# Kernel optimization log

Measured on AMD Instinct MI355X. Metric: run time of the kernel, lower is better.

The kernel has to match this reference:

```python
import jax, jax.numpy as jnp
import numpy as np

K = 3
STRIDE = 1
PAD = 1
DIL = 1


def conv2d(x, w, b, stride, pad, dil):
    y = jax.lax.conv_general_dilated(
        x, w, (stride, stride), [(pad, pad), (pad, pad)],
        rhs_dilation=(dil, dil), dimension_numbers=("NCHW", "OIHW", "NCHW"))
    return y + b[None, :, None, None]


def bilinear_gather(img, ys, xs):
    # img: (C,H,W); ys,xs: (KK,Ho,Wo) pixel coords.
    # grid_sample(mode=bilinear, padding_mode=zeros, align_corners=True):
    # out-of-range corners contribute 0, interpolation weights unchanged.
    H, W = img.shape[-2:]
    y0 = jnp.floor(ys)
    x0 = jnp.floor(xs)
    wy1 = ys - y0
    wx1 = xs - x0
    wy0 = 1.0 - wy1
    wx0 = 1.0 - wx1

    def g(yc, xc):
        yi = yc.astype(jnp.int32)
        xi = xc.astype(jnp.int32)
        valid = (yi >= 0) & (yi < H) & (xi >= 0) & (xi < W)
        yi = jnp.clip(yi, 0, H - 1)
        xi = jnp.clip(xi, 0, W - 1)
        v = img[:, yi, xi]  # (C,KK,Ho,Wo)
        return v * valid[None].astype(img.dtype)

    return (g(y0, x0) * (wy0 * wx0)[None]
            + g(y0, x0 + 1.0) * (wy0 * wx1)[None]
            + g(y0 + 1.0, x0) * (wy1 * wx0)[None]
            + g(y0 + 1.0, x0 + 1.0) * (wy1 * wx1)[None])


def setup_inputs() -> dict:
    key = jax.random.key(0)
    ks = jax.random.split(key, 4)
    B, C_in, H, W = 8, 64, 96, 96
    C_out = 64
    x = jax.random.normal(ks[0], (B, C_in, H, W), dtype=jnp.float32)
    weight = jax.random.normal(ks[1], (C_out, C_in, K, K), dtype=jnp.float32) * 0.05
    bias = jax.random.normal(ks[2], (C_out,), dtype=jnp.float32) * 0.01
    off_w = jax.random.normal(ks[3], (2 * K * K, C_in, K, K), dtype=jnp.float32) * 0.05
    off_b = jnp.zeros((2 * K * K,), dtype=jnp.float32)
    return {"x": x, "weight": weight, "bias": bias, "off_w": off_w, "off_b": off_b}


def reference(x, weight, bias, off_w, off_b):
    B, C, H, W = x.shape
    Ho = (H + 2 * PAD - DIL * (K - 1) - 1) // STRIDE + 1
    Wo = (W + 2 * PAD - DIL * (K - 1) - 1) // STRIDE + 1

    offsets = conv2d(x, off_w, off_b, STRIDE, PAD, DIL)  # (B,2*K*K,Ho,Wo)
    off = offsets.reshape(B, K * K, 2, Ho, Wo)

    # Base sampling grid (note: original code does NOT subtract padding; kept faithful).
    by, bx = jnp.meshgrid(jnp.arange(Ho, dtype=x.dtype), jnp.arange(Wo, dtype=x.dtype), indexing="ij")
    by = by * STRIDE + (K // 2) * DIL
    bx = bx * STRIDE + (K // 2) * DIL
    ko = jnp.arange(-(K // 2), K // 2 + 1, dtype=x.dtype)
    ky, kx = jnp.meshgrid(ko, ko, indexing="ij")

    sy = by[None, None] + ky.reshape(1, -1, 1, 1) + off[:, :, 0]  # (B,KK,Ho,Wo)
    sx = bx[None, None] + kx.reshape(1, -1, 1, 1) + off[:, :, 1]

    sampled = jax.vmap(bilinear_gather)(x, sy, sx)  # (B,C,KK,Ho,Wo)

    wflat = weight.reshape(weight.shape[0], C, K * K)  # (O,C,KK)
    out = jnp.einsum("bckhw,ock->bohw", sampled, wflat)
    return out + bias[None, :, None, None]
```

## Files before the change

### kernel.cpp

```cpp
#include <hip/hip_runtime.h>
#include <hip/hip_bf16.h>

#define HH 96
#define WW 96
#define HW 9216
#define NB 8

typedef __bf16 bf16x8 __attribute__((ext_vector_type(8)));
typedef float  f32x4  __attribute__((ext_vector_type(4)));

union BF8 { uint4 u; bf16x8 v; unsigned short s[8]; };

__device__ __forceinline__ unsigned short f2bf_bits(float f) {
    unsigned u = __float_as_uint(f);
    unsigned r = u + 0x7FFFu + ((u >> 16) & 1u);
    return (unsigned short)(r >> 16);
}
__device__ __forceinline__ float bf2f(unsigned short s) {
    return __uint_as_float(((unsigned)s) << 16);
}
__device__ __forceinline__ unsigned pkbf(float a, float b) {
    union { __hip_bfloat162 h; unsigned u; } c;
    c.h = __float22bfloat162_rn(make_float2(a, b));
    return c.u;
}

__device__ __forceinline__ void bl_setup(int h, int w, int r, int s, float oy, float ox,
                                         int* a, float* wg) {
    float sy = (float)(h + r) + oy;
    float sx = (float)(w + s) + ox;
    float fy = floorf(sy), fx = floorf(sx);
    int   y0 = (int)fy, x0 = (int)fx;
    int   y1 = y0 + 1, x1 = x0 + 1;
    float wy1 = sy - fy, wx1 = sx - fx;
    float wy0 = 1.f - wy1, wx0 = 1.f - wx1;
    float m00 = (y0 >= 0 && y0 < HH && x0 >= 0 && x0 < WW) ? 1.f : 0.f;
    float m01 = (y0 >= 0 && y0 < HH && x1 >= 0 && x1 < WW) ? 1.f : 0.f;
    float m10 = (y1 >= 0 && y1 < HH && x0 >= 0 && x0 < WW) ? 1.f : 0.f;
    float m11 = (y1 >= 0 && y1 < HH && x1 >= 0 && x1 < WW) ? 1.f : 0.f;
    int cy0 = min(max(y0, 0), HH - 1), cy1 = min(max(y1, 0), HH - 1);
    int cx0 = min(max(x0, 0), WW - 1), cx1 = min(max(x1, 0), WW - 1);
    a[0] = (cy0 * WW + cx0) * 64;  a[1] = (cy0 * WW + cx1) * 64;
    a[2] = (cy1 * WW + cx0) * 64;  a[3] = (cy1 * WW + cx1) * 64;
    wg[0] = wy0 * wx0 * m00;  wg[1] = wy0 * wx1 * m01;
    wg[2] = wy1 * wx0 * m10;  wg[3] = wy1 * wx1 * m11;
}

__global__ __launch_bounds__(256) void xcvt_prep(const float* __restrict__ x,
                                                 const float* __restrict__ weight,
                                                 const float* __restrict__ off_w,
                                                 unsigned short* __restrict__ xt,
                                                 unsigned short* __restrict__ wTb2,
                                                 unsigned short* __restrict__ owTb2) {
    __shared__ unsigned short T[64 * 64];
    int bid   = blockIdx.x;
    int t     = threadIdx.x;
    int b     = bid & 7;
    int pbase = (bid >> 3) * 64;
    int pl    = t & 63;
    int q     = t >> 6;

    const float* xp = x + ((size_t)(b * 64 + q * 16)) * HW + pbase + pl;
    unsigned short hb[16];
#pragma unroll
    for (int i = 0; i < 16; ++i) hb[i] = f2bf_bits(xp[(size_t)i * HW]);

    uint4 w0, w1;
    w0.x = hb[0]  | (hb[1]  << 16); w0.y = hb[2]  | (hb[3]  << 16);
    w0.z = hb[4]  | (hb[5]  << 16); w0.w = hb[6]  | (hb[7]  << 16);
    w1.x = hb[8]  | (hb[9]  << 16); w1.y = hb[10] | (hb[11] << 16);
    w1.z = hb[12] | (hb[13] << 16); w1.w = hb[14] | (hb[15] << 16);
    int sw = pl & 7;
    *(uint4*)&T[pl * 64 + (((2 * q)     ^ sw) << 3)] = w0;
    *(uint4*)&T[pl * 64 + (((2 * q + 1) ^ sw) << 3)] = w1;
    __syncthreads();

    int row = t >> 2, rs = row & 7;
    uint4 a  = *(const uint4*)&T[row * 64 + ((((t & 3) * 2)     ^ rs) << 3)];
    uint4 b2 = *(const uint4*)&T[row * 64 + ((((t & 3) * 2 + 1) ^ rs) << 3)];
    unsigned short* dst = xt + ((size_t)(b * HW + pbase)) * 64 + t * 16;
    *(uint4*)dst       = a;
    *(uint4*)(dst + 8) = b2;

    if (bid < 216) {
        int i = bid * 256 + t;
        if (i < 36864) {
            int ch = i & 7, lnn = (i >> 3) & 15, qdd = (i >> 7) & 3;
            int kc = (i >> 9) & 1, ct = (i >> 10) & 3, tap = i >> 12;
            int co = ct * 16 + lnn;
            int c  = kc * 32 + qdd * 8 + ch;
            wTb2[i] = f2bf_bits(weight[(co * 64 + c) * 9 + tap]);
        } else {
            int f = i - 36864;
            int ch = f & 7, lnn = (f >> 3) & 15, qdd = (f >> 7) & 3;
            int kc = (f >> 9) & 1, jt = (f >> 10) & 1, tap = f >> 11;
            int j = jt * 16 + lnn;
            int c = kc * 32 + qdd * 8 + ch;
            owTb2[f] = (j < 18) ? f2bf_bits(off_w[(j * 64 + c) * 9 + tap]) : (unsigned short)0;
        }
    }
}

__global__ __launch_bounds__(256) void deform_all(const unsigned short* __restrict__ xt,
                                                  const unsigned short* __restrict__ wTb2,
                                                  const unsigned short* __restrict__ owTb2,
                                                  const float* __restrict__ bias,
                                                  const float* __restrict__ ob,
                                                  float* __restrict__ out) {
    __shared__ float offs[4][16 * 20];

    int bid   = blockIdx.x;
    int t     = threadIdx.x;
    int b     = bid & 7;
    int wv    = t >> 6;
    int l     = t & 63;
    int ln    = l & 15;
    int qd    = l >> 4;
    int pbase = (bid >> 3) * 64 + wv * 16;
    int px    = pbase + ln;
    int h     = px / WW, w = px - h * WW;

    const unsigned short* xb = xt + (size_t)b * HW * 64;

    f32x4 aj0 = {0.f, 0.f, 0.f, 0.f};
    f32x4 aj1 = {0.f, 0.f, 0.f, 0.f};
#pragma unroll
    for (int tap = 0; tap < 9; ++tap) {
        int  r  = tap / 3, s = tap - r * 3;
        int  iy = h - 1 + r, ix = w - 1 + s;
        bool vd = (iy >= 0) & (iy < HH) & (ix >= 0) & (ix < WW);
        int  rec = (min(max(iy, 0), HH - 1) * WW + min(max(ix, 0), WW - 1)) * 64;
        BF8 a0, a1;
        a0.u = *(const uint4*)(xb + rec + qd * 8);
        a1.u = *(const uint4*)(xb + rec + 32 + qd * 8);
        if (!vd) { a0.u = make_uint4(0,0,0,0); a1.u = make_uint4(0,0,0,0); }

        const unsigned short* base0 = owTb2 + (size_t)tap * 2048 + l * 8;
        BF8 b00, b01, b10, b11;
        b00.u = *(const uint4*)(base0);
        b01.u = *(const uint4*)(base0 + 512);
        b10.u = *(const uint4*)(base0 + 1024);
        b11.u = *(const uint4*)(base0 + 1536);
        aj0 = __builtin_amdgcn_mfma_f32_16x16x32_bf16(a0.v, b00.v, aj0, 0, 0, 0);
        aj0 = __builtin_amdgcn_mfma_f32_16x16x32_bf16(a1.v, b01.v, aj0, 0, 0, 0);
        aj1 = __builtin_amdgcn_mfma_f32_16x16x32_bf16(a0.v, b10.v, aj1, 0, 0, 0);
        aj1 = __builtin_amdgcn_mfma_f32_16x16x32_bf16(a1.v, b11.v, aj1, 0, 0, 0);
    }

    {
        float* ow_ = offs[wv];
        float  obj = ob[ln];
#pragma unroll
        for (int rg = 0; rg < 4; ++rg) ow_[(qd * 4 + rg) * 20 + ln] = aj0[rg] + obj;
        if (ln < 2) {
            float obj1 = ob[16 + ln];
#pragma unroll
            for (int rg = 0; rg < 4; ++rg) ow_[(qd * 4 + rg) * 20 + 16 + ln] = aj1[rg] + obj1;
        }
    }
    float oy[9], ox[9];
#pragma unroll
    for (int k = 0; k < 9; ++k) {
        float2 p = *(const float2*)&offs[wv][ln * 20 + 2 * k];
        oy[k] = p.x; ox[k] = p.y;
    }

    f32x4 acc[4] = {{0.f,0.f,0.f,0.f},{0.f,0.f,0.f,0.f},{0.f,0.f,0.f,0.f},{0.f,0.f,0.f,0.f}};

#pragma unroll
    for (int tap = 0; tap < 9; ++tap) {
        int r = tap / 3, s = tap - r * 3;
        int   aa[4];
        float gg[4];
        bl_setup(h, w, r, s, oy[tap], ox[tap], aa, gg);

        BF8 f0[4], f1[4];
#pragma unroll
        for (int c = 0; c < 4; ++c) {
            f0[c].u = *(const uint4*)(xb + aa[c] + qd * 8);
            f1[c].u = *(const uint4*)(xb + aa[c] + 32 + qd * 8);
        }

        BF8 A0, A1;
        {
            float v0[8], v1[8];
#pragma unroll
            for (int i = 0; i < 8; ++i) {
                v0[i] = gg[0] * bf2f(f0[0].s[i]) + gg[1] * bf2f(f0[1].s[i])
                      + gg[2] * bf2f(f0[2].s[i]) + gg[3] * bf2f(f0[3].s[i]);
                v1[i] = gg[0] * bf2f(f1[0].s[i]) + gg[1] * bf2f(f1[1].s[i])
                      + gg[2] * bf2f(f1[2].s[i]) + gg[3] * bf2f(f1[3].s[i]);
            }
            A0.u.x = pkbf(v0[0], v0[1]); A0.u.y = pkbf(v0[2], v0[3]);
            A0.u.z = pkbf(v0[4], v0[5]); A0.u.w = pkbf(v0[6], v0[7]);
            A1.u.x = pkbf(v1[0], v1[1]); A1.u.y = pkbf(v1[2], v1[3]);
            A1.u.z = pkbf(v1[4], v1[5]); A1.u.w = pkbf(v1[6], v1[7]);
        }

        const unsigned short* wb = wTb2 + (size_t)tap * 4096 + l * 8;
#pragma unroll
        for (int ct = 0; ct < 4; ++ct) {
            BF8 B0, B1;
            B0.u = *(const uint4*)(wb + ct * 1024);
            B1.u = *(const uint4*)(wb + ct * 1024 + 512);
            acc[ct] = __builtin_amdgcn_mfma_f32_16x16x32_bf16(A0.v, B0.v, acc[ct], 0, 0, 0);
            acc[ct] = __builtin_amdgcn_mfma_f32_16x16x32_bf16(A1.v, B1.v, acc[ct], 0, 0, 0);
        }
    }

#pragma unroll
    for (int ct = 0; ct < 4; ++ct) {
        int   co = ct * 16 + ln;
        float bv = bias[co];
        float4 st;
        st.x = acc[ct][0] + bv; st.y = acc[ct][1] + bv;
        st.z = acc[ct][2] + bv; st.w = acc[ct][3] + bv;
        *(float4*)(out + ((size_t)(b * 64 + co)) * HW + pbase + qd * 4) = st;
    }
}

extern "C" void kernel_launch(void* const* d_in, const int* in_sizes, int n_in,
                              void* d_out, int out_size, void* d_ws, size_t ws_size,
                              hipStream_t stream) {
    const float* x      = (const float*)d_in[0];
    const float* weight = (const float*)d_in[1];
    const float* bias   = (const float*)d_in[2];
    const float* off_w  = (const float*)d_in[3];
    const float* off_b  = (const float*)d_in[4];
    float* out = (float*)d_out;

    unsigned short* xt    = (unsigned short*)d_ws;
    unsigned short* wTb2  = xt + 4718592;
    unsigned short* owTb2 = wTb2 + 36864;

    hipLaunchKernelGGL(xcvt_prep,  dim3(1152), dim3(256), 0, stream,
                       x, weight, off_w, xt, wTb2, owTb2);
    hipLaunchKernelGGL(deform_all, dim3(1152), dim3(256), 0, stream,
                       xt, wTb2, owTb2, bias, off_b, out);
}
```

Baseline: 145.3 us.

## Prefetch offset-conv inputs and double-buffer bilinear corner gathers across taps

Issues all nine offset-conv input loads up front, replacing the branch on out-of-range taps with a bitmask. All bilinear setups are precomputed, and corner gathers are software-pipelined two taps ahead through a two-slot register buffer, so memory latency overlaps the interpolation and MFMA work. Launch bounds now request 2 blocks per CU to cap registers. The much higher register footprint risks spills or lower occupancy.

```diff
diff --git a/kernel.cpp b/kernel.cpp
--- a/kernel.cpp
+++ b/kernel.cpp
@@ -101,12 +101,12 @@
     }
 }
 
-__global__ __launch_bounds__(256) void deform_all(const unsigned short* __restrict__ xt,
-                                                  const unsigned short* __restrict__ wTb2,
-                                                  const unsigned short* __restrict__ owTb2,
-                                                  const float* __restrict__ bias,
-                                                  const float* __restrict__ ob,
-                                                  float* __restrict__ out) {
+__global__ __launch_bounds__(256, 2) void deform_all(const unsigned short* __restrict__ xt,
+                                                     const unsigned short* __restrict__ wTb2,
+                                                     const unsigned short* __restrict__ owTb2,
+                                                     const float* __restrict__ bias,
+                                                     const float* __restrict__ ob,
+                                                     float* __restrict__ out) {
     __shared__ float offs[4][16 * 20];
 
     int bid   = blockIdx.x;
@@ -122,18 +122,28 @@
 
     const unsigned short* xb = xt + (size_t)b * HW * 64;
 
-    f32x4 aj0 = {0.f, 0.f, 0.f, 0.f};
-    f32x4 aj1 = {0.f, 0.f, 0.f, 0.f};
+    uint4 pa0[9], pa1[9];
+    int   vmsk[9];
 #pragma unroll
     for (int tap = 0; tap < 9; ++tap) {
         int  r  = tap / 3, s = tap - r * 3;
         int  iy = h - 1 + r, ix = w - 1 + s;
-        bool vd = (iy >= 0) & (iy < HH) & (ix >= 0) & (ix < WW);
+        vmsk[tap] = ((iy >= 0) & (iy < HH) & (ix >= 0) & (ix < WW)) ? -1 : 0;
         int  rec = (min(max(iy, 0), HH - 1) * WW + min(max(ix, 0), WW - 1)) * 64;
+        pa0[tap] = *(const uint4*)(xb + rec + qd * 8);
+        pa1[tap] = *(const uint4*)(xb + rec + 32 + qd * 8);
+    }
+
+    f32x4 aj0 = {0.f, 0.f, 0.f, 0.f};
+    f32x4 aj1 = {0.f, 0.f, 0.f, 0.f};
+#pragma unroll
+    for (int tap = 0; tap < 9; ++tap) {
+        unsigned m = (unsigned)vmsk[tap];
         BF8 a0, a1;
-        a0.u = *(const uint4*)(xb + rec + qd * 8);
-        a1.u = *(const uint4*)(xb + rec + 32 + qd * 8);
-        if (!vd) { a0.u = make_uint4(0,0,0,0); a1.u = make_uint4(0,0,0,0); }
+        a0.u.x = pa0[tap].x & m; a0.u.y = pa0[tap].y & m;
+        a0.u.z = pa0[tap].z & m; a0.u.w = pa0[tap].w & m;
+        a1.u.x = pa1[tap].x & m; a1.u.y = pa1[tap].y & m;
+        a1.u.z = pa1[tap].z & m; a1.u.w = pa1[tap].w & m;
 
         const unsigned short* base0 = owTb2 + (size_t)tap * 2048 + l * 8;
         BF8 b00, b01, b10, b11;
@@ -165,31 +175,44 @@
         oy[k] = p.x; ox[k] = p.y;
     }
 
+    int   aa[9][4];
+    float gg[9][4];
+#pragma unroll
+    for (int k = 0; k < 9; ++k) {
+        int r = k / 3, s = k - r * 3;
+        bl_setup(h, w, r, s, oy[k], ox[k], aa[k], gg[k]);
+    }
+
     f32x4 acc[4] = {{0.f,0.f,0.f,0.f},{0.f,0.f,0.f,0.f},{0.f,0.f,0.f,0.f},{0.f,0.f,0.f,0.f}};
 
-#pragma unroll
-    for (int tap = 0; tap < 9; ++tap) {
-        int r = tap / 3, s = tap - r * 3;
-        int   aa[4];
-        float gg[4];
-        bl_setup(h, w, r, s, oy[tap], ox[tap], aa, gg);
-
-        BF8 f0[4], f1[4];
-#pragma unroll
-        for (int c = 0; c < 4; ++c) {
-            f0[c].u = *(const uint4*)(xb + aa[c] + qd * 8);
-            f1[c].u = *(const uint4*)(xb + aa[c] + 32 + qd * 8);
-        }
+    uint4 cf0[2][4], cf1[2][4];
+#pragma unroll
+    for (int c = 0; c < 4; ++c) {
+        cf0[0][c] = *(const uint4*)(xb + aa[0][c] + qd * 8);
+        cf1[0][c] = *(const uint4*)(xb + aa[0][c] + 32 + qd * 8);
+    }
+#pragma unroll
+    for (int c = 0; c < 4; ++c) {
+        cf0[1][c] = *(const uint4*)(xb + aa[1][c] + qd * 8);
+        cf1[1][c] = *(const uint4*)(xb + aa[1][c] + 32 + qd * 8);
+    }
+
+#pragma unroll
+    for (int k = 0; k < 9; ++k) {
+        int slot = k & 1;
 
         BF8 A0, A1;
         {
+            BF8 q0, q1, q2, q3, r0, r1, r2, r3;
+            q0.u = cf0[slot][0]; q1.u = cf0[slot][1]; q2.u = cf0[slot][2]; q3.u = cf0[slot][3];
+            r0.u = cf1[slot][0]; r1.u = cf1[slot][1]; r2.u = cf1[slot][2]; r3.u = cf1[slot][3];
             float v0[8], v1[8];
 #pragma unroll
             for (int i = 0; i < 8; ++i) {
-                v0[i] = gg[0] * bf2f(f0[0].s[i]) + gg[1] * bf2f(f0[1].s[i])
-                      + gg[2] * bf2f(f0[2].s[i]) + gg[3] * bf2f(f0[3].s[i]);
-                v1[i] = gg[0] * bf2f(f1[0].s[i]) + gg[1] * bf2f(f1[1].s[i])
-                      + gg[2] * bf2f(f1[2].s[i]) + gg[3] * bf2f(f1[3].s[i]);
+                v0[i] = gg[k][0] * bf2f(q0.s[i]) + gg[k][1] * bf2f(q1.s[i])
+                      + gg[k][2] * bf2f(q2.s[i]) + gg[k][3] * bf2f(q3.s[i]);
+                v1[i] = gg[k][0] * bf2f(r0.s[i]) + gg[k][1] * bf2f(r1.s[i])
+                      + gg[k][2] * bf2f(r2.s[i]) + gg[k][3] * bf2f(r3.s[i]);
             }
             A0.u.x = pkbf(v0[0], v0[1]); A0.u.y = pkbf(v0[2], v0[3]);
             A0.u.z = pkbf(v0[4], v0[5]); A0.u.w = pkbf(v0[6], v0[7]);
@@ -197,7 +220,15 @@
             A1.u.z = pkbf(v1[4], v1[5]); A1.u.w = pkbf(v1[6], v1[7]);
         }
 
-        const unsigned short* wb = wTb2 + (size_t)tap * 4096 + l * 8;
+        if (k + 2 < 9) {
+#pragma unroll
+            for (int c = 0; c < 4; ++c) {
+                cf0[slot][c] = *(const uint4*)(xb + aa[k + 2][c] + qd * 8);
+                cf1[slot][c] = *(const uint4*)(xb + aa[k + 2][c] + 32 + qd * 8);
+            }
+        }
+
+        const unsigned short* wb = wTb2 + (size_t)k * 4096 + l * 8;
 #pragma unroll
         for (int ct = 0; ct < 4; ++ct) {
             BF8 B0, B1;
```

Result: no change. 145.5 us (+0.2%).
